# Kernel optimization log

Measured on AMD Instinct MI355X. Metric: run time of the kernel, lower is better.

## Reference

```python
import jax, jax.numpy as jnp
import numpy as np

LATENT, OBS, CTRL, SEQ = 2048, 1024, 512, 4096


def setup_inputs() -> dict:
    key = jax.random.key(0)
    k1, k2, k3, k4, k5 = jax.random.split(key, 5)
    inputs = jax.random.normal(k1, (OBS, SEQ), jnp.float32)
    controls = jax.random.normal(k2, (CTRL, SEQ), jnp.float32)
    # Weight matrices (init args A, B, C of the torch module)
    Wr = jax.random.normal(k3, (LATENT, LATENT), jnp.float32) * (0.9 / np.sqrt(LATENT))
    Win = jax.random.normal(k4, (LATENT, CTRL), jnp.float32) * (1.0 / np.sqrt(CTRL))
    Wout = jax.random.normal(k5, (OBS, LATENT), jnp.float32) * (1.0 / np.sqrt(LATENT))
    return {"inputs": inputs, "controls": controls, "Wr": Wr, "Win": Win,
            "Wout": Wout, "inf_iters": 20, "inf_lr": 0.05}


def reference(inputs, controls, Wr, Win, Wout, inf_iters, inf_lr):
    """NeuralKalmanFilter.predict with nonlin='tanh', dynamic_inf=False, inf_iters>0."""
    inf_lr = jnp.float32(inf_lr)

    def step(z, xu):
        x, u = xu  # x: (OBS,), u: (CTRL,)
        # z_proj uses prev_z (the carry before inference updates)
        drive = Wr @ jnp.tanh(z) + Win @ jnp.tanh(u)  # (LATENT,)

        def inf_body(_, z):
            fz = jnp.tanh(z)
            ez = z - drive
            ex = x - Wout @ fz             # x - pred_x
            dz = ez - (1.0 - fz * fz) * (Wout.T @ ex)
            return z - inf_lr * dz

        z = jax.lax.fori_loop(0, inf_iters, inf_body, z)
        return z, (z, drive)

    z0 = jnp.zeros((LATENT,), jnp.float32)
    _, (zs, z_projs) = jax.lax.scan(step, z0, (inputs.T, controls.T))
    zs = zs.T            # (LATENT, SEQ)
    z_projs = z_projs.T  # (LATENT, SEQ)
    pred_xs = Wout @ jnp.tanh(z_projs)  # (OBS, SEQ)
    return zs, pred_xs
```

## Files before the change

kernel.cpp:

```cpp
#include <hip/hip_runtime.h>


#define SEQL 4096
#define NLAT 2048
#define NOBS 1024
#define NCTL 512

typedef unsigned short u16;
typedef unsigned int   u32;
typedef unsigned long long u64;
typedef float v2f __attribute__((ext_vector_type(2)));

__device__ __forceinline__ float bfl(u32 u)  { return __uint_as_float(u << 16); }
__device__ __forceinline__ float bfh(u32 u)  { return __uint_as_float(u & 0xffff0000u); }
__device__ __forceinline__ float bf2f(u16 s) { return __uint_as_float(((u32)s) << 16); }
__device__ __forceinline__ u16 f2bf(float f) {
  u32 x = __float_as_uint(f);
  return (u16)((x + 0x7fffu + ((x >> 16) & 1u)) >> 16);
}
__device__ __forceinline__ float dq14(u32 u) {
  int q = ((int)(u << 18)) >> 18;
  return (float)q * 1.2208521548046392e-4f;
}

#if __has_builtin(__builtin_elementwise_fma)
__device__ __forceinline__ v2f pkfma(v2f a, v2f b, v2f c) {
  return __builtin_elementwise_fma(a, b, c);
}
#else
__device__ __forceinline__ v2f pkfma(v2f a, v2f b, v2f c) {
  v2f r; r.x = fmaf(a.x, b.x, c.x); r.y = fmaf(a.y, b.y, c.y); return r;
}
#endif

__device__ __forceinline__ float fast_tanh(float x) {
#if __has_builtin(__builtin_amdgcn_exp2f) && __has_builtin(__builtin_amdgcn_rcpf)
  float e = __builtin_amdgcn_exp2f(x * 2.8853900817779268f);
  return 1.f - 2.f * __builtin_amdgcn_rcpf(e + 1.f);
#else
  return tanhf(x);
#endif
}

template <int CTRL>
__device__ __forceinline__ float dpp_add(float x) {
#if __has_builtin(__builtin_amdgcn_update_dpp)
  int y = __builtin_amdgcn_update_dpp(0, __float_as_int(x), CTRL, 0xF, 0xF, true);
  return x + __int_as_float(y);
#else
  return x + __shfl_xor(x, (CTRL == 0xB1) ? 1 : 2, 64);
#endif
}
__device__ __forceinline__ float red32(float x) {
  x = dpp_add<0xB1>(x);
  x = dpp_add<0x4E>(x);
  x += __shfl_xor(x, 4, 64);
  x += __shfl_xor(x, 8, 64);
  x += __shfl_xor(x, 16, 64);
  return x;
}

__device__ __forceinline__ u64 LDW(const u64* p) {
  return __hip_atomic_load(p, __ATOMIC_RELAXED, __HIP_MEMORY_SCOPE_AGENT);
}

__global__ void k_f2b(const float* __restrict__ in, u16* __restrict__ out, int n) {
  int i = blockIdx.x * 256 + threadIdx.x;
  if (i < n) out[i] = f2bf(in[i]);
}
__global__ void k_tanh2b(const float* __restrict__ in, u16* __restrict__ out, int n) {
  int i = blockIdx.x * 256 + threadIdx.x;
  if (i < n) out[i] = f2bf(tanhf(in[i]));
}
__global__ void k_tr2b(const float* __restrict__ in, u16* __restrict__ out, int R, int C) {
  int i = blockIdx.x * 256 + threadIdx.x;
  if (i < R * C) {
    int r = i / C, c = i % C;
    out[(size_t)c * R + r] = f2bf(in[i]);
  }
}
__global__ void k_zero(u64* __restrict__ p, int n) {
  int i = blockIdx.x * 256 + threadIdx.x;
  if (i < n) p[i] = 0ull;
}

__global__ __launch_bounds__(256) void gemm_bf16(
    const u16* __restrict__ A, const u16* __restrict__ B,
    float* __restrict__ Cf, u16* __restrict__ Cb, int M, int N, int K)
{
  __shared__ float As[32][68];
  __shared__ float Bs[32][68];
  const int tid = threadIdx.x;
  const int colBase = blockIdx.x * 64, rowBase = blockIdx.y * 64;
  const int tx = tid & 15, ty = tid >> 4;
  const int ar = tid >> 2, ak = (tid & 3) * 8;
  const int bk = tid >> 3, bc = (tid & 7) * 8;
  const u16* Ap = A + (size_t)(rowBase + ar) * K + ak;
  const u16* Bp = B + (size_t)bk * N + colBase + bc;
  float acc[4][4] = {};

  for (int k0 = 0; k0 < K; k0 += 32) {
    uint4 a = *(const uint4*)(Ap + k0);
    uint4 b = *(const uint4*)(Bp + (size_t)k0 * N);
    As[ak + 0][ar] = bfl(a.x); As[ak + 1][ar] = bfh(a.x);
    As[ak + 2][ar] = bfl(a.y); As[ak + 3][ar] = bfh(a.y);
    As[ak + 4][ar] = bfl(a.z); As[ak + 5][ar] = bfh(a.z);
    As[ak + 6][ar] = bfl(a.w); As[ak + 7][ar] = bfh(a.w);
    Bs[bk][bc + 0] = bfl(b.x); Bs[bk][bc + 1] = bfh(b.x);
    Bs[bk][bc + 2] = bfl(b.y); Bs[bk][bc + 3] = bfh(b.y);
    Bs[bk][bc + 4] = bfl(b.z); Bs[bk][bc + 5] = bfh(b.z);
    Bs[bk][bc + 6] = bfl(b.w); Bs[bk][bc + 7] = bfh(b.w);
    __syncthreads();
#pragma unroll
    for (int kk = 0; kk < 32; kk++) {
      float4 av = *(const float4*)&As[kk][ty * 4];
      float4 bv = *(const float4*)&Bs[kk][tx * 4];
      float a4[4] = {av.x, av.y, av.z, av.w};
      float b4[4] = {bv.x, bv.y, bv.z, bv.w};
#pragma unroll
      for (int i = 0; i < 4; i++)
#pragma unroll
        for (int q = 0; q < 4; q++)
          acc[i][q] = fmaf(a4[i], b4[q], acc[i][q]);
    }
    __syncthreads();
  }

  if (Cf) {
#pragma unroll
    for (int i = 0; i < 4; i++) {
      float4 v = make_float4(acc[i][0], acc[i][1], acc[i][2], acc[i][3]);
      *(float4*)&Cf[(size_t)(rowBase + ty * 4 + i) * N + colBase + tx * 4] = v;
    }
  } else {
#pragma unroll
    for (int i = 0; i < 4; i++) {
      u64 pk = (u64)f2bf(acc[i][0]) | ((u64)f2bf(acc[i][1]) << 16) |
               ((u64)f2bf(acc[i][2]) << 32) | ((u64)f2bf(acc[i][3]) << 48);
      *(u64*)&Cb[(size_t)(rowBase + ty * 4 + i) * N + colBase + tx * 4] = pk;
    }
  }
}

__global__ void __launch_bounds__(256, 1)
scan_kernel(const u16* __restrict__ G,
            const u16* __restrict__ Wr,
            const u16* __restrict__ Bmat,
            const u16* __restrict__ Cin,
            float* __restrict__ zs,
            u16* __restrict__ td,
            u64* __restrict__ fzbuf,
            const int* __restrict__ itp, const float* __restrict__ lrp)
{
  __shared__ __align__(16) float fzL[2][NLAT];
  __shared__ u64 hand[4];
  __shared__ int sAbort;

  const int tid = threadIdx.x, bid = blockIdx.x;
  const int lane = tid & 63, wv = tid >> 6;
  const int h = lane >> 5;
  const int chunk = lane & 31;
  const int myrow = (bid << 3) + (wv << 1) + h;

  const int niters = *itp;
  const float lr = *lrp;

  uint2 wGp[16], wWp[16];
  {
    const u16* gRow = G  + (size_t)myrow * NLAT + chunk * 4;
    const u16* wRow = Wr + (size_t)myrow * NLAT + chunk * 4;
#pragma unroll
    for (int i = 0; i < 16; i++) {
      wGp[i] = *(const uint2*)(gRow + 128 * i);
      wWp[i] = *(const uint2*)(wRow + 128 * i);
    }
  }
  for (int i = tid; i < 2 * NLAT; i += 256) (&fzL[0][0])[i] = 0.f;
  if (tid < 4) hand[tid] = 0ull;
  if (tid == 0) sAbort = 0;

  const int w0 = tid, w1 = tid + 256;
  const bool sk0 = (w0 >> 1) == bid, sk1 = (w1 >> 1) == bid;

  float z = 0.f, fz = 0.f, drive = 0.f, bv = 0.f;
  float bvN = bf2f(Bmat[(size_t)myrow * SEQL]);
  float cvN = bf2f(Cin [(size_t)myrow * SEQL]);
  __syncthreads();

  u32 p = 0;
  for (int t = 0; t < SEQL; t++) {
    for (int j = 0; j < niters; j++) {
      p++;
      const int wb = p & 1, rb = wb ^ 1;
      v2f aG0 = {0.f,0.f}, aG1 = {0.f,0.f}, aG2 = {0.f,0.f}, aG3 = {0.f,0.f};
      const float4* f4 = (const float4*)(&fzL[rb][chunk * 4]);
      float accW = 0.f;
      if (j == 0) {
        v2f aW0 = {0.f,0.f}, aW1 = {0.f,0.f};
#pragma unroll
        for (int i = 0; i < 16; i += 2) {
          float4 va = f4[32 * i], vb = f4[32 * (i + 1)];
          uint2 ga = wGp[i], gb = wGp[i + 1];
          uint2 wa = wWp[i], wbm = wWp[i + 1];
          v2f va0 = {va.x, va.y}, va1 = {va.z, va.w};
          v2f vb0 = {vb.x, vb.y}, vb1 = {vb.z, vb.w};
          aG0 = pkfma((v2f){bfl(ga.x), bfh(ga.x)}, va0, aG0);
          aG1 = pkfma((v2f){bfl(ga.y), bfh(ga.y)}, va1, aG1);
          aG2 = pkfma((v2f){bfl(gb.x), bfh(gb.x)}, vb0, aG2);
          aG3 = pkfma((v2f){bfl(gb.y), bfh(gb.y)}, vb1, aG3);
          aW0 = pkfma((v2f){bfl(wa.x), bfh(wa.x)}, va0, aW0);
          aW0 = pkfma((v2f){bfl(wa.y), bfh(wa.y)}, va1, aW0);
          aW1 = pkfma((v2f){bfl(wbm.x), bfh(wbm.x)}, vb0, aW1);
          aW1 = pkfma((v2f){bfl(wbm.y), bfh(wbm.y)}, vb1, aW1);
        }
        v2f aW = aW0 + aW1;
        accW = red32(aW.x + aW.y);
      } else {
#pragma unroll
        for (int i = 0; i < 16; i += 2) {
          float4 va = f4[32 * i], vb = f4[32 * (i + 1)];
          uint2 ga = wGp[i], gb = wGp[i + 1];
          aG0 = pkfma((v2f){bfl(ga.x), bfh(ga.x)}, (v2f){va.x, va.y}, aG0);
          aG1 = pkfma((v2f){bfl(ga.y), bfh(ga.y)}, (v2f){va.z, va.w}, aG1);
          aG2 = pkfma((v2f){bfl(gb.x), bfh(gb.x)}, (v2f){vb.x, vb.y}, aG2);
          aG3 = pkfma((v2f){bfl(gb.y), bfh(gb.y)}, (v2f){vb.z, vb.w}, aG3);
        }
      }
      v2f aG = (aG0 + aG1) + (aG2 + aG3);
      float accG = red32(aG.x + aG.y);

      if (j == 0) { bv = bvN; drive = accW + cvN; }
      float corr = bv - accG;
      float dz = (z - drive) - (1.f - fz * fz) * corr;
      z -= lr * dz;
      fz = fast_tanh(z);

      const u32 tag8 = p & 0xffu;
      int qi = (int)rintf(fz * 8191.f);
      u32 uq = (u32)qi & 0x3FFFu;
      u32 oq = (u32)__shfl_xor((int)uq, 32, 64) & 0x3FFFu;
      if (lane == 0) {
        u64 wd = ((u64)(tag8 | (oq << 8)) << 32) | (u64)(tag8 | (uq << 8));
        __hip_atomic_store(&hand[wv], wd, __ATOMIC_RELAXED,
                           __HIP_MEMORY_SCOPE_WORKGROUP);
      }
      asm volatile("" ::: "memory");

      if (wv == 0) {
        for (;;) {
          u64 hv = __hip_atomic_load(&hand[lane & 3], __ATOMIC_RELAXED,
                                     __HIP_MEMORY_SCOPE_WORKGROUP);
          bool ok = (((u32)hv & 0xffu) == tag8) && (((u32)(hv >> 32) & 0xffu) == tag8);
          if (__all(ok)) break;
        }
        if (lane < 16) {
          int rep = lane >> 1, k = lane & 1;
          u64 ha = __hip_atomic_load(&hand[2 * k], __ATOMIC_RELAXED,
                                     __HIP_MEMORY_SCOPE_WORKGROUP);
          u64 hb = __hip_atomic_load(&hand[2 * k + 1], __ATOMIC_RELAXED,
                                     __HIP_MEMORY_SCOPE_WORKGROUP);
          u64 q0 = ((u32)ha >> 8) & 0x3FFFu;
          u64 q1 = ((u32)(ha >> 32) >> 8) & 0x3FFFu;
          u64 q2 = ((u32)hb >> 8) & 0x3FFFu;
          u64 q3 = ((u32)(hb >> 32) >> 8) & 0x3FFFu;
          u64 word = (u64)tag8 | (q0 << 8) | (q1 << 22) | (q2 << 36) | (q3 << 50);
          __hip_atomic_store(fzbuf + ((size_t)wb * 8 + rep) * 512 + (bid << 1) + k,
                             word, __ATOMIC_RELAXED, __HIP_MEMORY_SCOPE_AGENT);
        }
        if (lane < 4) {
          u64 ha = __hip_atomic_load(&hand[lane], __ATOMIC_RELAXED,
                                     __HIP_MEMORY_SCOPE_WORKGROUP);
          ((float2*)fzL[wb])[(bid << 2) + lane] =
              make_float2(dq14((u32)ha >> 8), dq14((u32)(ha >> 32) >> 8));
        }
      }

      const u64* base = fzbuf + ((size_t)wb * 8 + (bid & 7)) * 512;
      u64 g0 = LDW(base + w0), g1 = LDW(base + w1);

      if (j == 0) {
        if (chunk == 0) td[(size_t)myrow * SEQL + t] = f2bf(fast_tanh(drive));
        int tn = t + 1 < SEQL ? t + 1 : t;
        bvN = bf2f(Bmat[(size_t)myrow * SEQL + tn]);
        cvN = bf2f(Cin [(size_t)myrow * SEQL + tn]);
      }
      if (j == niters - 1 && chunk == 0) zs[(size_t)myrow * SEQL + t] = z;

      int guard = 0;
      for (;;) {
        bool bad0 = !sk0 && ((u32)g0 & 0xffu) != tag8;
        bool bad1 = !sk1 && ((u32)g1 & 0xffu) != tag8;
        if (!(bad0 || bad1)) break;
        if (++guard > 150000) { sAbort = 1; break; }
        if (bad0) g0 = LDW(base + w0);
        if (bad1) g1 = LDW(base + w1);
#if __has_builtin(__builtin_amdgcn_s_sleep)
        __builtin_amdgcn_s_sleep(1);
#endif
      }

      if (!sk0)
        *(float4*)&fzL[wb][w0 << 2] =
            make_float4(dq14((u32)(g0 >> 8)),  dq14((u32)(g0 >> 22)),
                        dq14((u32)(g0 >> 36)), dq14((u32)(g0 >> 50)));
      if (!sk1)
        *(float4*)&fzL[wb][w1 << 2] =
            make_float4(dq14((u32)(g1 >> 8)),  dq14((u32)(g1 >> 22)),
                        dq14((u32)(g1 >> 36)), dq14((u32)(g1 >> 50)));
      __syncthreads();
      if (sAbort) return;
    }
  }
}

extern "C" void kernel_launch(void* const* d_in, const int* in_sizes, int n_in,
                              void* d_out, int out_size, void* d_ws, size_t ws_size,
                              hipStream_t stream)
{
  const float* inputs   = (const float*)d_in[0];
  const float* controls = (const float*)d_in[1];
  const float* Wr       = (const float*)d_in[2];
  const float* Win      = (const float*)d_in[3];
  const float* Wout     = (const float*)d_in[4];
  const int*   itp      = (const int*)d_in[5];
  const float* lrp      = (const float*)d_in[6];
  float* out = (float*)d_out;
  char* ws = (char*)d_ws;

  size_t off = 0;
  u16*   WrB   = (u16*)(ws + off);   off += (size_t)NLAT * NLAT * 2;
  u16*   Gb    = (u16*)(ws + off);   off += (size_t)NLAT * NLAT * 2;
  u16*   WoutB = (u16*)(ws + off);   off += (size_t)NOBS * NLAT * 2;
  u16*   WinB  = (u16*)(ws + off);   off += (size_t)NLAT * NCTL * 2;
  u16*   XB    = (u16*)(ws + off);   off += (size_t)NOBS * SEQL * 2;
  u16*   UB    = (u16*)(ws + off);   off += (size_t)NCTL * SEQL * 2;
  u16*   WoutT = (u16*)(ws + off);   off += (size_t)NLAT * NOBS * 2;
  u16*   CinB  = (u16*)(ws + off);   off += (size_t)NLAT * SEQL * 2;
  u16*   TD    = (u16*)(ws + off);   off += (size_t)NLAT * SEQL * 2;
  u64*   fzbuf = (u64*)(ws + off);   off += (size_t)2 * 8 * 512 * 8;

  float* zs   = out;
  float* pred = out + (size_t)NLAT * SEQL;
  u16* BmatB  = (u16*)pred;

  k_f2b   <<<(NLAT * NLAT + 255) / 256, 256, 0, stream>>>(Wr,    WrB,   NLAT * NLAT);
  k_f2b   <<<(NOBS * NLAT + 255) / 256, 256, 0, stream>>>(Wout,  WoutB, NOBS * NLAT);
  k_f2b   <<<(NLAT * NCTL + 255) / 256, 256, 0, stream>>>(Win,   WinB,  NLAT * NCTL);
  k_f2b   <<<(NOBS * SEQL + 255) / 256, 256, 0, stream>>>(inputs, XB,   NOBS * SEQL);
  k_tanh2b<<<(NCTL * SEQL + 255) / 256, 256, 0, stream>>>(controls, UB, NCTL * SEQL);
  k_tr2b  <<<(NOBS * NLAT + 255) / 256, 256, 0, stream>>>(Wout, WoutT, NOBS, NLAT);
  k_zero  <<<(2 * 8 * 512 + 255) / 256, 256, 0, stream>>>(fzbuf, 2 * 8 * 512);

  gemm_bf16<<<dim3(NLAT / 64, NLAT / 64), 256, 0, stream>>>(WoutT, WoutB, nullptr, Gb,
                                                            NLAT, NLAT, NOBS);
  gemm_bf16<<<dim3(SEQL / 64, NLAT / 64), 256, 0, stream>>>(WoutT, XB, nullptr, BmatB,
                                                            NLAT, SEQL, NOBS);
  gemm_bf16<<<dim3(SEQL / 64, NLAT / 64), 256, 0, stream>>>(WinB, UB, nullptr, CinB,
                                                            NLAT, SEQL, NCTL);

  const u16* Gc = Gb; const u16* Wrc = WrB; const u16* Bc = BmatB; const u16* Cc = CinB;
  float* zsp = zs; u16* tdp = TD; u64* fzp = fzbuf;
  const int* it = itp; const float* lr = lrp;
  void* args[9] = { &Gc, &Wrc, &Bc, &Cc, &zsp, &tdp, &fzp, &it, &lr };
  hipLaunchCooperativeKernel((void*)scan_kernel, dim3(NLAT / 8), dim3(256), args, 0, stream);

  gemm_bf16<<<dim3(SEQL / 64, NOBS / 64), 256, 0, stream>>>(WoutB, TD, pred, nullptr,
                                                            NOBS, SEQL, NLAT);
}
```

Baseline: 185.4 ms.

## Pair waves to publish fz words directly instead of single gatherer wave

Each even wave now waits only on its odd mate's handoff slot and publishes the combined 4-value quantized word to the global fzbuf replicas and local fzL itself. Previously wave 0 waited for all four waves and then published for everyone. This shortens the intra-block critical path in the per-iteration cross-block exchange. The publishing wave temporarily raises its scheduling priority, and the first polling retries skip s_sleep to cut latency, at the cost of somewhat more spinning traffic.

```diff
diff --git a/kernel.cpp b/kernel.cpp
--- a/kernel.cpp
+++ b/kernel.cpp
@@ -161,6 +161,9 @@
   const int h = lane >> 5;
   const int chunk = lane & 31;
   const int myrow = (bid << 3) + (wv << 1) + h;
+  const bool isPub = (wv & 1) == 0;
+  const int mate = wv | 1;
+  const int kw = wv >> 1;
 
   const int niters = *itp;
   const float lr = *lrp;
@@ -239,40 +242,36 @@
       int qi = (int)rintf(fz * 8191.f);
       u32 uq = (u32)qi & 0x3FFFu;
       u32 oq = (u32)__shfl_xor((int)uq, 32, 64) & 0x3FFFu;
-      if (lane == 0) {
-        u64 wd = ((u64)(tag8 | (oq << 8)) << 32) | (u64)(tag8 | (uq << 8));
-        __hip_atomic_store(&hand[wv], wd, __ATOMIC_RELAXED,
-                           __HIP_MEMORY_SCOPE_WORKGROUP);
-      }
-      asm volatile("" ::: "memory");
-
-      if (wv == 0) {
+      if (!isPub) {
+        if (lane == 0) {
+          u64 wd = ((u64)(tag8 | (oq << 8)) << 32) | (u64)(tag8 | (uq << 8));
+          __hip_atomic_store(&hand[wv], wd, __ATOMIC_RELAXED,
+                             __HIP_MEMORY_SCOPE_WORKGROUP);
+        }
+      } else {
+#if __has_builtin(__builtin_amdgcn_s_setprio)
+        __builtin_amdgcn_s_setprio(1);
+#endif
+        u64 hv;
         for (;;) {
-          u64 hv = __hip_atomic_load(&hand[lane & 3], __ATOMIC_RELAXED,
-                                     __HIP_MEMORY_SCOPE_WORKGROUP);
-          bool ok = (((u32)hv & 0xffu) == tag8) && (((u32)(hv >> 32) & 0xffu) == tag8);
-          if (__all(ok)) break;
+          hv = __hip_atomic_load(&hand[mate], __ATOMIC_RELAXED,
+                                 __HIP_MEMORY_SCOPE_WORKGROUP);
+          if ((((u32)hv & 0xffu) == tag8) &&
+              (((u32)(hv >> 32) & 0xffu) == tag8)) break;
         }
-        if (lane < 16) {
-          int rep = lane >> 1, k = lane & 1;
-          u64 ha = __hip_atomic_load(&hand[2 * k], __ATOMIC_RELAXED,
-                                     __HIP_MEMORY_SCOPE_WORKGROUP);
-          u64 hb = __hip_atomic_load(&hand[2 * k + 1], __ATOMIC_RELAXED,
-                                     __HIP_MEMORY_SCOPE_WORKGROUP);
-          u64 q0 = ((u32)ha >> 8) & 0x3FFFu;
-          u64 q1 = ((u32)(ha >> 32) >> 8) & 0x3FFFu;
-          u64 q2 = ((u32)hb >> 8) & 0x3FFFu;
-          u64 q3 = ((u32)(hb >> 32) >> 8) & 0x3FFFu;
-          u64 word = (u64)tag8 | (q0 << 8) | (q1 << 22) | (q2 << 36) | (q3 << 50);
-          __hip_atomic_store(fzbuf + ((size_t)wb * 8 + rep) * 512 + (bid << 1) + k,
+        u64 q2 = ((u32)hv >> 8) & 0x3FFFu;
+        u64 q3 = ((u32)(hv >> 32) >> 8) & 0x3FFFu;
+        u64 word = (u64)tag8 | ((u64)uq << 8) | ((u64)oq << 22) | (q2 << 36) | (q3 << 50);
+        if (lane < 8)
+          __hip_atomic_store(fzbuf + ((size_t)wb * 8 + lane) * 512 + (bid << 1) + kw,
                              word, __ATOMIC_RELAXED, __HIP_MEMORY_SCOPE_AGENT);
-        }
-        if (lane < 4) {
-          u64 ha = __hip_atomic_load(&hand[lane], __ATOMIC_RELAXED,
-                                     __HIP_MEMORY_SCOPE_WORKGROUP);
-          ((float2*)fzL[wb])[(bid << 2) + lane] =
-              make_float2(dq14((u32)ha >> 8), dq14((u32)(ha >> 32) >> 8));
-        }
+        else if (lane == 8)
+          *(float4*)&fzL[wb][((bid << 1) + kw) << 2] =
+              make_float4(dq14((u32)(word >> 8)),  dq14((u32)(word >> 22)),
+                          dq14((u32)(word >> 36)), dq14((u32)(word >> 50)));
+#if __has_builtin(__builtin_amdgcn_s_setprio)
+        __builtin_amdgcn_s_setprio(0);
+#endif
       }
 
       const u64* base = fzbuf + ((size_t)wb * 8 + (bid & 7)) * 512;
@@ -295,7 +294,7 @@
         if (bad0) g0 = LDW(base + w0);
         if (bad1) g1 = LDW(base + w1);
 #if __has_builtin(__builtin_amdgcn_s_sleep)
-        __builtin_amdgcn_s_sleep(1);
+        if (guard >= 2) __builtin_amdgcn_s_sleep(1);
 #endif
       }
 
```

Measured after the change: 247.0 ms. +33.2%, slower.
